# Performance work log

Hardware: AMD Instinct MI355X
Metric: run time of the kernel (lower is better)

The kernel has to match this reference:

```python
import jax, jax.numpy as jnp
import numpy as np
import math

N, D, E, M, MODS = 16384, 1024, 5, 64, 5
K = 1  # top-k for sparse router


def setup_inputs() -> dict:
    key = jax.random.key(0)
    ks = jax.random.split(key, 24)
    rn = lambda k, shape, s=1.0: jax.random.normal(k, shape, dtype=jnp.float32) * s
    inp = {
        'x': rn(ks[0], (N, D)),
        'spectrogram': rn(ks[1], (N, D)),
        'waveform': rn(ks[2], (N, D)),
        'pitch': rn(ks[3], (N, D)),
        'envelope': rn(ks[4], (N, D)),
        'phase': rn(ks[5], (N, D)),
        # routers (torch Linear: y = x @ W.T + b, W is [out,in]); init std=0.01
        'Wsoft': rn(ks[6], (E, D), 0.01), 'bsoft': jnp.zeros((E,), jnp.float32),
        'Wsparse': rn(ks[7], (E, D), 0.01), 'bsparse': jnp.zeros((E,), jnp.float32),
        # memory (plain randn, not re-initialized)
        'm_key': rn(ks[8], (M, D)), 'm_val': rn(ks[9], (M, E)),
        # experts: Linear(D,D) -> SiLU -> Linear(D,D), stacked over E
        'W1': rn(ks[10], (E, D, D), 0.01), 'b1': jnp.zeros((E, D), jnp.float32),
        'W2': rn(ks[11], (E, D, D), 0.01), 'b2': jnp.zeros((E, D), jnp.float32),
        # fusion gates: Linear(D,1) + sigmoid, one per modality
        'Wg': rn(ks[12], (MODS, D), 0.01), 'bg': jnp.zeros((MODS,), jnp.float32),
        # fusion projection: Linear(D*MODS, D)
        'Wf': rn(ks[13], (D, D * MODS), 0.01), 'bf': jnp.zeros((D,), jnp.float32),
    }
    return inp


def reference(x, spectrogram, waveform, pitch, envelope, phase,
              Wsoft, bsoft, Wsparse, bsparse, m_key, m_val,
              W1, b1, W2, b2, Wg, bg, Wf, bf):
    alpha_moe = jnp.float32(0.5)
    alpha_fusion = jnp.float32(0.5)

    # soft router: softmax(Linear)
    soft_w = jax.nn.softmax(x @ Wsoft.T + bsoft, axis=-1)          # [N,E]

    # sparse router: top-k + softmax, scattered back to [N,E]
    logits = x @ Wsparse.T + bsparse                               # [N,E]
    top_vals, top_idx = jax.lax.top_k(logits, K)                   # [N,K]
    sparse_gates = jax.nn.softmax(top_vals, axis=-1)               # [N,K]
    one_hot = jax.nn.one_hot(top_idx, E, dtype=logits.dtype)       # [N,K,E]
    sparse_w = jnp.sum(one_hot * sparse_gates[..., None], axis=1)  # [N,E]

    # memory-augmented gating
    attn = jax.nn.softmax((x @ m_key.T) / math.sqrt(D), axis=-1)   # [N,M]
    memory_w = jax.nn.softmax(attn @ m_val, axis=-1)               # [N,E]

    mixed_w = alpha_moe * sparse_w + (1 - alpha_moe) * soft_w
    final_w = (mixed_w + memory_w) / 2                             # [N,E]

    # dense all-expert MLP: [N,E,D]
    h = jax.nn.silu(jnp.einsum('nd,eod->neo', x, W1) + b1)
    expert_out = jnp.einsum('ned,eod->neo', h, W2) + b2
    moe_output = jnp.einsum('neo,ne->no', expert_out, final_w)     # [N,D]

    # gated multimodal fusion
    features = [spectrogram, waveform, pitch, envelope, phase]
    gates = jax.nn.sigmoid(x @ Wg.T + bg)                          # [N,MODS]
    scaled = [gates[:, q:q + 1] * features[q] for q in range(MODS)]
    fused = jnp.concatenate(scaled, axis=-1) @ Wf.T + bf           # [N,D]

    return alpha_fusion * fused + (1 - alpha_fusion) * moe_output
```

## Files before the change

kernel.cpp:

```cpp
#include <hip/hip_runtime.h>
#include <stdint.h>

typedef __bf16 bf16x8 __attribute__((ext_vector_type(8)));
typedef float f32x4 __attribute__((ext_vector_type(4)));
typedef unsigned short u16;
typedef u16 ushort8 __attribute__((ext_vector_type(8)));
typedef u16 ushort4v __attribute__((ext_vector_type(4)));

__device__ __forceinline__ u16 f2bf(float f) {
    uint32_t u = __builtin_bit_cast(uint32_t, f);
    u += 0x7FFFu + ((u >> 16) & 1u);
    return (u16)(u >> 16);
}

__device__ __forceinline__ void gload16(const void* g, void* l) {
    __builtin_amdgcn_global_load_lds(
        reinterpret_cast<const __attribute__((address_space(1))) void*>(reinterpret_cast<uintptr_t>(g)),
        reinterpret_cast<__attribute__((address_space(3))) void*>(reinterpret_cast<uintptr_t>(l)),
        16, 0, 0);
}

#define BAR() asm volatile("s_barrier" ::: "memory")

template <int MODE>
__global__ __launch_bounds__(512, 2)
void gemm256(const u16* __restrict__ A, int lda,
             const u16* __restrict__ B, int ldb, int K,
             void* __restrict__ Cout, int ldc,
             const float* __restrict__ bias, const float* __restrict__ fw05,
             const float* __restrict__ g05,
             const float* __restrict__ f0, const float* __restrict__ f1,
             const float* __restrict__ f2, const float* __restrict__ f3,
             const float* __restrict__ f4)
{
    __shared__ __align__(16) u16 As[2 * 256 * 64];
    __shared__ __align__(16) u16 Bs[2 * 256 * 64];

    const int t    = threadIdx.x;
    const int lane = t & 63;
    const int wave = t >> 6;
    const int l16  = lane & 15;
    const int lhi  = lane >> 4;
    const int wm   = wave >> 2;
    const int wn   = wave & 3;

    const int gx  = gridDim.x;
    const int nwg = gx * gridDim.y;
    int id  = blockIdx.y * gx + blockIdx.x;
    int swz = (nwg & 7) ? id : ((id & 7) * (nwg >> 3) + (id >> 3));
    const int bx = swz % gx;
    const int by = swz / gx;

    const size_t rowBase = (size_t)by * 256;
    const int    colBase = bx * 256;
    const int    NT      = K >> 6;

    const int rl0 = t >> 3;
    const int ko0 = (t & 7) * 8;
    const int kos = ((t & 7) ^ (rl0 & 7)) * 8;

    const u16* aRow = A + (rowBase + rl0) * (size_t)lda + kos;
    const u16* bRow = B + (size_t)(colBase + rl0) * ldb + kos;
    u16* asW = As + rl0 * 64 + ko0;
    u16* bsW = Bs + rl0 * 64 + ko0;

#define STA(bufo, e, r0, r1)                                                     \
    do {                                                                         \
        gload16(aRow + (size_t)(r0) * lda + (e), asW + (bufo) + (r0) * 64);      \
        gload16(aRow + (size_t)(r1) * lda + (e), asW + (bufo) + (r1) * 64);      \
    } while (0)
#define STB(bufo, e, b0)                                                         \
    do {                                                                         \
        gload16(bRow + (size_t)(b0) * ldb + (e), bsW + (bufo) + (b0) * 64);      \
        gload16(bRow + (size_t)((b0) + 64) * ldb + (e),                          \
                bsW + (bufo) + ((b0) + 64) * 64);                                \
    } while (0)

    const int sw = l16 & 7;
    const u16* aRd0 = As + (wm * 128 + l16) * 64 + ((lhi ^ sw) * 8);
    const u16* aRd1 = As + (wm * 128 + l16) * 64 + (((lhi + 4) ^ sw) * 8);
    const u16* bRd0 = Bs + (wn * 64 + l16) * 64 + ((lhi ^ sw) * 8);
    const u16* bRd1 = Bs + (wn * 64 + l16) * 64 + (((lhi + 4) ^ sw) * 8);

#define RDAF(dst, cc, qq)                                                        \
    do {                                                                         \
        dst[0][0] = *(const bf16x8*)(aRd0 + (cc) + (2 * (qq) + 0) * 1024);       \
        dst[0][1] = *(const bf16x8*)(aRd1 + (cc) + (2 * (qq) + 0) * 1024);       \
        dst[1][0] = *(const bf16x8*)(aRd0 + (cc) + (2 * (qq) + 1) * 1024);       \
        dst[1][1] = *(const bf16x8*)(aRd1 + (cc) + (2 * (qq) + 1) * 1024);       \
    } while (0)

#define MM(af, r0)                                                               \
    do {                                                                         \
        __builtin_amdgcn_s_setprio(1);                                           \
        _Pragma("unroll")                                                        \
        for (int s = 0; s < 2; ++s)                                              \
            _Pragma("unroll")                                                    \
            for (int ni = 0; ni < 4; ++ni)                                       \
                _Pragma("unroll")                                                \
                for (int kk = 0; kk < 2; ++kk)                                   \
                    acc[(r0) + s][ni] = __builtin_amdgcn_mfma_f32_16x16x32_bf16( \
                        af[s][kk], bfr[ni][kk], acc[(r0) + s][ni], 0, 0, 0);     \
        __builtin_amdgcn_s_setprio(0);                                           \
    } while (0)

    f32x4 acc[8][4];
#pragma unroll
    for (int i = 0; i < 8; i++)
#pragma unroll
        for (int j = 0; j < 4; j++)
            acc[i][j] = (f32x4){0.f, 0.f, 0.f, 0.f};

    const float* fsrc = nullptr;
    int   dbase = 0;
    f32x4 bl0 = {0.f, 0.f, 0.f, 0.f}, bl1 = {0.f, 0.f, 0.f, 0.f};
    float bgd = 0.f;
    if constexpr (MODE == 0) {
        const int qm = bx >> 2;
        fsrc  = (qm == 0) ? f0 : (qm == 1) ? f1 : (qm == 2) ? f2 : (qm == 3) ? f3 : f4;
        dbase = (bx & 3) * 256;
        const int br = t >> 5, bc = (t & 31) * 8;
        bl0 = *(const f32x4*)(fsrc + (rowBase + br) * 1024 + dbase + bc);
        bl1 = *(const f32x4*)(fsrc + (rowBase + br) * 1024 + dbase + bc + 4);
        bgd = g05[(rowBase + br) * 5 + (bx >> 2)];
    }

    STA(0, 0, 0, 128);
    STA(0, 0, 64, 192);
    STB(0, 0, 0);
    STB(0, 0, 128);
    const int e1p = (NT > 1) ? 64 : 0;
    STB(16384, e1p, 0);
    STB(16384, e1p, 128);
    STA(16384, e1p, 0, 128);
    asm volatile("s_waitcnt vmcnt(6)" ::: "memory");
    BAR();

    bf16x8 afA[2][2], afB[2][2], bfr[4][2];
    for (int tt = 0; tt < NT; ++tt) {
        const int c  = (tt & 1) << 14;
        const int cn = c ^ 16384;
        const int e1 = ((tt + 1 < NT) ? tt + 1 : NT - 1) << 6;
        const int e2 = ((tt + 2 < NT) ? tt + 2 : NT - 1) << 6;

        if constexpr (MODE == 0) {
            if (tt < 16) {
                const int idx = tt * 512 + t;
                const int br  = idx >> 5;
                const int bc  = (idx & 31) * 8;
                ushort8 bv;
                bv[0] = f2bf(bgd * bl0[0]); bv[1] = f2bf(bgd * bl0[1]);
                bv[2] = f2bf(bgd * bl0[2]); bv[3] = f2bf(bgd * bl0[3]);
                bv[4] = f2bf(bgd * bl1[0]); bv[5] = f2bf(bgd * bl1[1]);
                bv[6] = f2bf(bgd * bl1[2]); bv[7] = f2bf(bgd * bl1[3]);
                *(ushort8*)((u16*)Cout + (rowBase + br) * (size_t)ldc
                            + 5184 + colBase + bc) = bv;
                if (tt + 1 < 16) {
                    const int idx2 = (tt + 1) * 512 + t;
                    const int br2  = idx2 >> 5;
                    const int bc2  = (idx2 & 31) * 8;
                    bl0 = *(const f32x4*)(fsrc + (rowBase + br2) * 1024 + dbase + bc2);
                    bl1 = *(const f32x4*)(fsrc + (rowBase + br2) * 1024 + dbase + bc2 + 4);
                    bgd = g05[(rowBase + br2) * 5 + (bx >> 2)];
                }
            }
        }
        RDAF(afA, c, 0);
#pragma unroll
        for (int ni = 0; ni < 4; ++ni) {
            bfr[ni][0] = *(const bf16x8*)(bRd0 + c + ni * 16 * 64);
            bfr[ni][1] = *(const bf16x8*)(bRd1 + c + ni * 16 * 64);
        }
        STA(cn, e1, 64, 192);
        BAR();
        RDAF(afB, c, 1);
        MM(afA, 0);
        BAR();
        STB(c, e2, 0);
        BAR();
        RDAF(afA, c, 2);
        MM(afB, 2);
        BAR();
        STB(c, e2, 128);
        BAR();
        RDAF(afB, c, 3);
        MM(afA, 4);
        BAR();
        STA(c, e2, 0, 128);
        BAR();
        MM(afB, 6);
        asm volatile("s_waitcnt vmcnt(6)" ::: "memory");
        BAR();
    }

    const int orow = wm * 128 + lhi * 4;
    const int ocol = colBase + wn * 64 + l16;

    if constexpr (MODE == 0) {
        u16* C = (u16*)Cout;
        const int eidx = colBase >> 10;
#pragma unroll
        for (int mi = 0; mi < 8; mi++) {
#pragma unroll
            for (int j = 0; j < 4; j++) {
                size_t r = rowBase + orow + mi * 16 + j;
                float w = fw05[r * 5 + eidx];
#pragma unroll
                for (int ni = 0; ni < 4; ni++) {
                    int cc = ocol + ni * 16;
                    float v = acc[mi][ni][j] + bias[cc];
                    float s = v / (1.f + __expf(-v));
                    C[r * (size_t)ldc + cc] = f2bf(w * s);
                }
            }
        }
    } else {
        float* C = (float*)Cout;
#pragma unroll
        for (int mi = 0; mi < 8; mi++) {
#pragma unroll
            for (int j = 0; j < 4; j++) {
                size_t r = rowBase + orow + mi * 16 + j;
#pragma unroll
                for (int ni = 0; ni < 4; ni++) {
                    size_t idx = r * (size_t)ldc + (ocol + ni * 16);
                    C[idx] = acc[mi][ni][j];
                }
            }
        }
    }
#undef STA
#undef STB
#undef RDAF
#undef MM
}

__global__ __launch_bounds__(256)
void router_kernel(const float* __restrict__ x,
                   const float* __restrict__ Wsoft, const float* __restrict__ Wsparse,
                   const float* __restrict__ m_key, const float* __restrict__ Wg,
                   float* __restrict__ logits, u16* __restrict__ Xbf)
{
    __shared__ float Xs[128][66];
    __shared__ float Ws[80][132];

    const int t    = threadIdx.x;
    const int lane = t & 63;
    const int wave = t >> 6;
    const int row0 = blockIdx.x * 64;

    float acc[20];
#pragma unroll
    for (int c = 0; c < 20; c++) acc[c] = 0.f;

    for (int k0 = 0; k0 < 1024; k0 += 128) {
#pragma unroll
        for (int i = 0; i < 8; i++) {
            int f4 = i * 256 + t;
            int r  = f4 >> 5;
            int kk = (f4 & 31) * 4;
            f32x4 v = *(const f32x4*)(x + (size_t)(row0 + r) * 1024 + k0 + kk);
            Xs[kk + 0][r] = v[0]; Xs[kk + 1][r] = v[1];
            Xs[kk + 2][r] = v[2]; Xs[kk + 3][r] = v[3];
            ushort4v o4;
            o4[0] = f2bf(v[0]); o4[1] = f2bf(v[1]);
            o4[2] = f2bf(v[2]); o4[3] = f2bf(v[3]);
            *(ushort4v*)(Xbf + (size_t)(row0 + r) * 1024 + k0 + kk) = o4;
        }
#pragma unroll
        for (int i = 0; i < 10; i++) {
            int f4 = i * 256 + t;
            int j  = f4 >> 5;
            int kk = (f4 & 31) * 4;
            const float* src;
            if      (j < 5)  src = Wsoft   + (size_t)j * 1024;
            else if (j < 10) src = Wsparse + (size_t)(j - 5) * 1024;
            else if (j < 74) src = m_key   + (size_t)(j - 10) * 1024;
            else             src = Wg      + (size_t)(j - 74) * 1024;
            *(f32x4*)&Ws[j][kk] = *(const f32x4*)(src + k0 + kk);
        }
        __syncthreads();

        for (int k4 = 0; k4 < 32; k4++) {
            float x0 = Xs[k4 * 4 + 0][lane];
            float x1 = Xs[k4 * 4 + 1][lane];
            float x2 = Xs[k4 * 4 + 2][lane];
            float x3 = Xs[k4 * 4 + 3][lane];
#pragma unroll
            for (int c = 0; c < 20; c++) {
                f32x4 w = *(const f32x4*)&Ws[wave * 20 + c][k4 * 4];
                acc[c] += x0 * w[0] + x1 * w[1] + x2 * w[2] + x3 * w[3];
            }
        }
        __syncthreads();
    }

    float* dst = logits + (size_t)(row0 + lane) * 80 + wave * 20;
#pragma unroll
    for (int c = 0; c < 20; c++) dst[c] = acc[c];
}

__global__ __launch_bounds__(256)
void finalize_kernel(const float* __restrict__ logits, const float* __restrict__ m_val,
                     const float* __restrict__ bsoft, const float* __restrict__ bsparse,
                     const float* __restrict__ bg,
                     float* __restrict__ fw05, float* __restrict__ g05,
                     u16* __restrict__ Abuf, int NC)
{
    __shared__ float mv[320];
    for (int i = threadIdx.x; i < 320; i += 256) mv[i] = m_val[i];
    __syncthreads();

    int idx = blockIdx.x * 256 + threadIdx.x;
    if (idx >= NC) return;
    const float* L = logits + (size_t)idx * 80;

    float sl[5];
#pragma unroll
    for (int e = 0; e < 5; e++) sl[e] = L[e] + bsoft[e];
    float sm = sl[0];
#pragma unroll
    for (int e = 1; e < 5; e++) sm = fmaxf(sm, sl[e]);
    float ssum = 0.f, sw[5];
#pragma unroll
    for (int e = 0; e < 5; e++) { sw[e] = __expf(sl[e] - sm); ssum += sw[e]; }
    float sinv = 1.f / ssum;

    int am = 0; float bv = L[5] + bsparse[0];
#pragma unroll
    for (int e = 1; e < 5; e++) {
        float v = L[5 + e] + bsparse[e];
        if (v > bv) { bv = v; am = e; }
    }

    float amax = -1e30f;
    for (int m = 0; m < 64; m++) amax = fmaxf(amax, L[10 + m] * 0.03125f);
    float asum = 0.f, mw[5] = {0.f, 0.f, 0.f, 0.f, 0.f};
    for (int m = 0; m < 64; m++) {
        float a = __expf(L[10 + m] * 0.03125f - amax);
        asum += a;
#pragma unroll
        for (int e = 0; e < 5; e++) mw[e] += a * mv[m * 5 + e];
    }
    float ainv = 1.f / asum;
#pragma unroll
    for (int e = 0; e < 5; e++) mw[e] *= ainv;
    float mm = mw[0];
#pragma unroll
    for (int e = 1; e < 5; e++) mm = fmaxf(mm, mw[e]);
    float msum = 0.f, me[5];
#pragma unroll
    for (int e = 0; e < 5; e++) { me[e] = __expf(mw[e] - mm); msum += me[e]; }
    float minv = 1.f / msum;

    u16* ta = Abuf + (size_t)idx * 10368;
#pragma unroll
    for (int e = 0; e < 5; e++) {
        float fv = 0.125f * ((e == am) ? 1.f : 0.f) + 0.125f * sw[e] * sinv
                 + 0.25f * me[e] * minv;
        fw05[(size_t)idx * 5 + e] = fv;
        ta[5120 + e] = f2bf(fv);
    }
#pragma unroll
    for (int q = 0; q < 5; q++)
        g05[(size_t)idx * 5 + q] = 0.5f / (1.f + __expf(-(L[74 + q] + bg[q])));

    for (int j = 5125; j < 5184; j++) ta[j] = 0;
    ta[10304] = f2bf(0.5f);
    for (int j = 10305; j < 10368; j++) ta[j] = 0;
}

__global__ __launch_bounds__(256)
void cast_bf16_kernel(const float* __restrict__ src, u16* __restrict__ dst, size_t n)
{
    size_t i = ((size_t)blockIdx.x * 256 + threadIdx.x) * 8;
    if (i >= n) return;
    f32x4 a = *(const f32x4*)(src + i);
    f32x4 b = *(const f32x4*)(src + i + 4);
    ushort8 o;
    o[0] = f2bf(a[0]); o[1] = f2bf(a[1]); o[2] = f2bf(a[2]); o[3] = f2bf(a[3]);
    o[4] = f2bf(b[0]); o[5] = f2bf(b[1]); o[6] = f2bf(b[2]); o[7] = f2bf(b[3]);
    *(ushort8*)(dst + i) = o;
}

__global__ __launch_bounds__(256)
void prep_wcat(const float* __restrict__ W2, const float* __restrict__ b2,
               const float* __restrict__ Wf, const float* __restrict__ bfias,
               u16* __restrict__ out)
{
    size_t tid = (size_t)blockIdx.x * 256 + threadIdx.x;
    int o  = (int)(tid / 1296);
    int c0 = (int)(tid % 1296) * 8;
    ushort8 v;
    if (c0 + 8 <= 5120) {
        int e = c0 >> 10, d = c0 & 1023;
        const float* s = W2 + ((size_t)e * 1024 + o) * 1024 + d;
        f32x4 a = *(const f32x4*)s;
        f32x4 b = *(const f32x4*)(s + 4);
        v[0] = f2bf(a[0]); v[1] = f2bf(a[1]); v[2] = f2bf(a[2]); v[3] = f2bf(a[3]);
        v[4] = f2bf(b[0]); v[5] = f2bf(b[1]); v[6] = f2bf(b[2]); v[7] = f2bf(b[3]);
    } else if (c0 < 5184) {
#pragma unroll
        for (int jj = 0; jj < 8; jj++) {
            int c = c0 + jj;
            float f = (c >= 5120 && c < 5125) ? b2[(size_t)(c - 5120) * 1024 + o] : 0.f;
            v[jj] = f2bf(f);
        }
    } else {
        int c2 = c0 - 5184;
        if (c2 + 8 <= 5120) {
            const float* s = Wf + (size_t)o * 5120 + c2;
            f32x4 a = *(const f32x4*)s;
            f32x4 b = *(const f32x4*)(s + 4);
            v[0] = f2bf(a[0]); v[1] = f2bf(a[1]); v[2] = f2bf(a[2]); v[3] = f2bf(a[3]);
            v[4] = f2bf(b[0]); v[5] = f2bf(b[1]); v[6] = f2bf(b[2]); v[7] = f2bf(b[3]);
        } else {
#pragma unroll
            for (int jj = 0; jj < 8; jj++) {
                int cj = c2 + jj;
                v[jj] = f2bf((cj == 5120) ? bfias[o] : 0.f);
            }
        }
    }
    *(ushort8*)(out + (size_t)o * 10368 + c0) = v;
}

extern "C" void kernel_launch(void* const* d_in, const int* in_sizes, int n_in,
                              void* d_out, int out_size, void* d_ws, size_t ws_size,
                              hipStream_t stream)
{
    (void)in_sizes; (void)n_in; (void)out_size;

    const float* x      = (const float*)d_in[0];
    const float* spect  = (const float*)d_in[1];
    const float* wavef  = (const float*)d_in[2];
    const float* pitch  = (const float*)d_in[3];
    const float* envel  = (const float*)d_in[4];
    const float* phase  = (const float*)d_in[5];
    const float* Wsoft  = (const float*)d_in[6];
    const float* bsoft  = (const float*)d_in[7];
    const float* Wsparse= (const float*)d_in[8];
    const float* bsparse= (const float*)d_in[9];
    const float* m_key  = (const float*)d_in[10];
    const float* m_val  = (const float*)d_in[11];
    const float* W1     = (const float*)d_in[12];
    const float* b1     = (const float*)d_in[13];
    const float* W2     = (const float*)d_in[14];
    const float* b2     = (const float*)d_in[15];
    const float* Wg     = (const float*)d_in[16];
    const float* bg     = (const float*)d_in[17];
    const float* Wf     = (const float*)d_in[18];
    const float* bfias  = (const float*)d_in[19];
    float* out = (float*)d_out;

    const int N = 16384;

    size_t fixed = (size_t)5 * 1024 * 1024 * 2 + (size_t)1024 * 10368 * 2;
    int NC = 16384;
    while (NC > 256 && fixed + (size_t)NC * 23144 > ws_size) NC >>= 1;

    char* p = (char*)d_ws;
    u16* W1bf = (u16*)p; p += (size_t)5 * 1024 * 1024 * 2;
    u16* Wcat = (u16*)p; p += (size_t)1024 * 10368 * 2;
    u16* Xbf  = (u16*)p; p += (size_t)NC * 1024 * 2;
    u16* Abuf = (u16*)p; p += (size_t)NC * 10368 * 2;
    float* logits = (float*)p; p += (size_t)NC * 80 * 4;
    float* fw05   = (float*)p; p += (size_t)NC * 5 * 4;
    float* g05    = (float*)p; p += (size_t)NC * 5 * 4;

    cast_bf16_kernel<<<2560, 256, 0, stream>>>(W1, W1bf, (size_t)5 * 1024 * 1024);
    prep_wcat<<<5184, 256, 0, stream>>>(W2, b2, Wf, bfias, Wcat);

    for (int n0 = 0; n0 < N; n0 += NC) {
        const size_t off = (size_t)n0 * 1024;

        router_kernel<<<NC / 64, 256, 0, stream>>>(x + off, Wsoft, Wsparse, m_key, Wg,
                                                   logits, Xbf);
        finalize_kernel<<<(NC + 255) / 256, 256, 0, stream>>>(
            logits, m_val, bsoft, bsparse, bg, fw05, g05, Abuf, NC);

        gemm256<0><<<dim3(20, NC / 256), 512, 0, stream>>>(
            Xbf, 1024, W1bf, 1024, 1024, Abuf, 10368, b1, fw05, g05,
            spect + off, wavef + off, pitch + off, envel + off, phase + off);

        gemm256<1><<<dim3(4, NC / 256), 512, 0, stream>>>(
            Abuf, 10368, Wcat, 10368, 10368, out + off, 1024,
            nullptr, nullptr, nullptr, nullptr, nullptr, nullptr, nullptr, nullptr);
    }
}
```

Measured before the change: 683.0 us.

## Restructure GEMM main loop with sched_group_barrier interleaving and fewer barriers

Rewrites the GEMM inner loop so that global-to-LDS loads, LDS fragment reads and MFMAs are interleaved within each phase using sched_group_barrier hints, and cuts the number of s_barriers per iteration from eight to four. The next tile's first A fragments and B fragments are prefetched at the end of each iteration. The MODE 0 epilogue side-stream is made branch-free by clamping its index, so the last stores are rewritten redundantly. This hides LDS and VMEM latency behind matrix ops but depends on the adjusted vmcnt waits and barrier placement being correct for the double buffer.

```diff
diff --git a/kernel.cpp b/kernel.cpp
--- a/kernel.cpp
+++ b/kernel.cpp
@@ -21,6 +21,26 @@
 }
 
 #define BAR() asm volatile("s_barrier" ::: "memory")
+#define SGBi(m, n) __builtin_amdgcn_sched_group_barrier((m), (n), 0)
+
+template <int V>
+__device__ __forceinline__ void sgb_q() {
+    SGBi(0x70, V);
+    SGBi(0x8, 2); SGBi(0x100, 1);
+    SGBi(0x8, 2); SGBi(0x100, 1);
+    SGBi(0x8, 2); SGBi(0x100, 1);
+    SGBi(0x8, 2); SGBi(0x100, 1);
+    SGBi(0x8, 8);
+}
+__device__ __forceinline__ void sgb_q3() {
+    SGBi(0x70, 2);
+    SGBi(0x8, 1); SGBi(0x100, 1);
+    SGBi(0x8, 1); SGBi(0x100, 1);
+    SGBi(0x8, 1); SGBi(0x100, 1);
+    SGBi(0x8, 1); SGBi(0x100, 1);
+    SGBi(0x8, 12);
+    SGBi(0x100, 8);
+}
 
 template <int MODE>
 __global__ __launch_bounds__(512, 2)
@@ -89,8 +109,15 @@
         dst[1][0] = *(const bf16x8*)(aRd0 + (cc) + (2 * (qq) + 1) * 1024);       \
         dst[1][1] = *(const bf16x8*)(aRd1 + (cc) + (2 * (qq) + 1) * 1024);       \
     } while (0)
-
-#define MM(af, r0)                                                               \
+#define RDB(cc)                                                                  \
+    do {                                                                         \
+        _Pragma("unroll")                                                        \
+        for (int ni = 0; ni < 4; ++ni) {                                         \
+            bfr[ni][0] = *(const bf16x8*)(bRd0 + (cc) + ni * 1024);              \
+            bfr[ni][1] = *(const bf16x8*)(bRd1 + (cc) + ni * 1024);              \
+        }                                                                        \
+    } while (0)
+#define MMX(af, r0)                                                              \
     do {                                                                         \
         __builtin_amdgcn_s_setprio(1);                                           \
         _Pragma("unroll")                                                        \
@@ -129,14 +156,16 @@
     STA(0, 0, 64, 192);
     STB(0, 0, 0);
     STB(0, 0, 128);
-    const int e1p = (NT > 1) ? 64 : 0;
-    STB(16384, e1p, 0);
-    STB(16384, e1p, 128);
-    STA(16384, e1p, 0, 128);
+    STB(16384, 64, 0);
+    STB(16384, 64, 128);
+    STA(16384, 64, 0, 128);
     asm volatile("s_waitcnt vmcnt(6)" ::: "memory");
     BAR();
 
     bf16x8 afA[2][2], afB[2][2], bfr[4][2];
+    RDAF(afA, 0, 0);
+    RDB(0);
+
     for (int tt = 0; tt < NT; ++tt) {
         const int c  = (tt & 1) << 14;
         const int cn = c ^ 16384;
@@ -144,52 +173,48 @@
         const int e2 = ((tt + 2 < NT) ? tt + 2 : NT - 1) << 6;
 
         if constexpr (MODE == 0) {
-            if (tt < 16) {
-                const int idx = tt * 512 + t;
-                const int br  = idx >> 5;
-                const int bc  = (idx & 31) * 8;
-                ushort8 bv;
-                bv[0] = f2bf(bgd * bl0[0]); bv[1] = f2bf(bgd * bl0[1]);
-                bv[2] = f2bf(bgd * bl0[2]); bv[3] = f2bf(bgd * bl0[3]);
-                bv[4] = f2bf(bgd * bl1[0]); bv[5] = f2bf(bgd * bl1[1]);
-                bv[6] = f2bf(bgd * bl1[2]); bv[7] = f2bf(bgd * bl1[3]);
-                *(ushort8*)((u16*)Cout + (rowBase + br) * (size_t)ldc
-                            + 5184 + colBase + bc) = bv;
-                if (tt + 1 < 16) {
-                    const int idx2 = (tt + 1) * 512 + t;
-                    const int br2  = idx2 >> 5;
-                    const int bc2  = (idx2 & 31) * 8;
-                    bl0 = *(const f32x4*)(fsrc + (rowBase + br2) * 1024 + dbase + bc2);
-                    bl1 = *(const f32x4*)(fsrc + (rowBase + br2) * 1024 + dbase + bc2 + 4);
-                    bgd = g05[(rowBase + br2) * 5 + (bx >> 2)];
-                }
-            }
-        }
-        RDAF(afA, c, 0);
-#pragma unroll
-        for (int ni = 0; ni < 4; ++ni) {
-            bfr[ni][0] = *(const bf16x8*)(bRd0 + c + ni * 16 * 64);
-            bfr[ni][1] = *(const bf16x8*)(bRd1 + c + ni * 16 * 64);
+            const int idx = tt * 512 + t;
+            const int br  = idx >> 5;
+            const int bc  = (idx & 31) * 8;
+            ushort8 bv;
+            bv[0] = f2bf(bgd * bl0[0]); bv[1] = f2bf(bgd * bl0[1]);
+            bv[2] = f2bf(bgd * bl0[2]); bv[3] = f2bf(bgd * bl0[3]);
+            bv[4] = f2bf(bgd * bl1[0]); bv[5] = f2bf(bgd * bl1[1]);
+            bv[6] = f2bf(bgd * bl1[2]); bv[7] = f2bf(bgd * bl1[3]);
+            *(ushort8*)((u16*)Cout + (rowBase + br) * (size_t)ldc
+                        + 5184 + colBase + bc) = bv;
+            const int t2   = (tt + 1 < 16) ? tt + 1 : 15;
+            const int idx2 = t2 * 512 + t;
+            const int br2  = idx2 >> 5;
+            const int bc2  = (idx2 & 31) * 8;
+            bl0 = *(const f32x4*)(fsrc + (rowBase + br2) * 1024 + dbase + bc2);
+            bl1 = *(const f32x4*)(fsrc + (rowBase + br2) * 1024 + dbase + bc2 + 4);
+            bgd = g05[(rowBase + br2) * 5 + (bx >> 2)];
         }
         STA(cn, e1, 64, 192);
+        RDAF(afB, c, 1);
+        MMX(afA, 0);
+        sgb_q<(MODE == 0) ? 6 : 2>();
         BAR();
-        RDAF(afB, c, 1);
-        MM(afA, 0);
+
+        STB(c, e2, 0);
+        RDAF(afA, c, 2);
+        MMX(afB, 2);
+        sgb_q<2>();
         BAR();
-        STB(c, e2, 0);
+
+        STB(c, e2, 128);
+        RDAF(afB, c, 3);
+        MMX(afA, 4);
+        sgb_q<2>();
+        asm volatile("s_waitcnt vmcnt(4)" ::: "memory");
         BAR();
-        RDAF(afA, c, 2);
-        MM(afB, 2);
-        BAR();
-        STB(c, e2, 128);
-        BAR();
-        RDAF(afB, c, 3);
-        MM(afA, 4);
-        BAR();
+
         STA(c, e2, 0, 128);
-        BAR();
-        MM(afB, 6);
-        asm volatile("s_waitcnt vmcnt(6)" ::: "memory");
+        RDAF(afA, cn, 0);
+        MMX(afB, 6);
+        RDB(cn);
+        sgb_q3();
         BAR();
     }
 
@@ -232,7 +257,8 @@
 #undef STA
 #undef STB
 #undef RDAF
-#undef MM
+#undef RDB
+#undef MMX
 }
 
 __global__ __launch_bounds__(256)
```

New measurement: 665.7 us (median of 2 runs). 2.5% less time.
